# Kernel optimization log

Hardware: AMD Instinct MI355X
Metric: run time of the kernel (lower is better)

Reference implementation:

```python
import jax, jax.numpy as jnp
import numpy as np

FORGET_BIAS = 1.0  # TF BasicLSTMCell default


def _lstm_scan(xs, kernel, bias):
    """xs: [T, B, D]; kernel: [D+H, 4H]; bias: [4H]. Returns hs: [T, B, H]."""
    hidden = bias.shape[0] // 4
    batch = xs.shape[1]

    def step(carry, x):
        c, h = carry
        z = jnp.concatenate([x, h], axis=-1) @ kernel + bias
        i, j, f, o = jnp.split(z, 4, axis=-1)  # TF gate order: input, candidate, forget, output
        c_new = c * jax.nn.sigmoid(f + FORGET_BIAS) + jax.nn.sigmoid(i) * jnp.tanh(j)
        h_new = jnp.tanh(c_new) * jax.nn.sigmoid(o)
        return (c_new, h_new), h_new

    init = (jnp.zeros((batch, hidden), xs.dtype), jnp.zeros((batch, hidden), xs.dtype))
    _, hs = jax.lax.scan(step, init, xs)
    return hs


def setup_inputs() -> dict:
    key = jax.random.key(0)
    ks = jax.random.split(key, 8)
    B, T, D, H, V, L = 128, 512, 128, 128, 50000, 19
    return {
        "input_ids": jax.random.randint(ks[0], (B, T), 0, V, dtype=jnp.int32),
        "embedding_table": jax.random.normal(ks[1], (V, D), jnp.float32) * 0.02,
        "fw_kernel": jax.random.normal(ks[2], (D + H, 4 * H), jnp.float32) * 0.05,
        "fw_bias": jnp.zeros((4 * H,), jnp.float32),
        "bw_kernel": jax.random.normal(ks[3], (D + H, 4 * H), jnp.float32) * 0.05,
        "bw_bias": jnp.zeros((4 * H,), jnp.float32),
        "att_w": jax.random.normal(ks[4], (H,), jnp.float32) * 0.1,
        "fc_w": jax.random.normal(ks[5], (H, L), jnp.float32) * 0.1,
        "fc_b": jnp.zeros((L,), jnp.float32),
    }


def reference(input_ids, embedding_table, fw_kernel, fw_bias, bw_kernel, bw_bias, att_w, fc_w, fc_b):
    # Embedding lookup: [B, T, D]
    x = embedding_table[input_ids]
    xs = jnp.transpose(x, (1, 0, 2))  # [T, B, D] time-major for scan

    fw = jnp.transpose(_lstm_scan(xs, fw_kernel, fw_bias), (1, 0, 2))           # [B, T, H]
    bw = jnp.transpose(_lstm_scan(xs[::-1], bw_kernel, bw_bias)[::-1], (1, 0, 2))  # [B, T, H]

    Hsum = fw + bw                         # [B, T, H]
    M = jnp.tanh(Hsum)
    scores = jnp.einsum('bth,h->bt', M, att_w)
    alpha = jax.nn.softmax(scores, axis=-1)            # [B, T]
    r = jnp.einsum('bth,bt->bh', Hsum, alpha)          # attention-pooled [B, H]
    h_star = jnp.tanh(r)                               # keep_prob=1.0 -> dropout is identity

    logits = h_star @ fc_w + fc_b                      # [B, L]
    probabilities = jnp.argmax(jax.nn.softmax(logits, axis=-1), axis=1)
    predict_label_ids = jnp.argmax(logits, axis=1)
    l2_loss = 0.5 * (jnp.sum(fc_w * fc_w) + jnp.sum(fc_b * fc_b))  # tf.nn.l2_loss
    return logits, predict_label_ids, l2_loss, probabilities
```

## Files before the change

### kernel.cpp

```cpp
#include <hip/hip_runtime.h>

typedef unsigned short u16;
typedef unsigned int u32;
typedef short short8 __attribute__((ext_vector_type(8)));
typedef float f32x4 __attribute__((ext_vector_type(4)));

#define T_LEN 512
#define NCLS 19

#define L2E 1.4426950408889634f
#define TL2E 2.8853901617765067f

static __device__ __forceinline__ u16 f2bf(float f) {
  u32 u = __float_as_uint(f);
  u32 r = (u + 0x7FFFu + ((u >> 16) & 1u)) >> 16;
  return (u16)r;
}
static __device__ __forceinline__ float bf2f(u16 h) {
  return __uint_as_float(((u32)h) << 16);
}
static __device__ __forceinline__ float rcp_f(float x) { return __builtin_amdgcn_rcpf(x); }
static __device__ __forceinline__ float ex2(float x) { return __builtin_amdgcn_exp2f(x); }

__global__ __launch_bounds__(256) void k_embed(const int* __restrict__ ids,
                                               const float* __restrict__ table,
                                               u16* __restrict__ xs) {
  int i = blockIdx.x * 256 + threadIdx.x;
  int e = i * 4;
  int m = e >> 7;
  int col = e & 127;
  int t = m >> 7, b = m & 127;
  int id = ids[b * T_LEN + t];
  float4 v = *(const float4*)(table + (size_t)id * 128 + col);
  ushort4 o;
  o.x = f2bf(v.x); o.y = f2bf(v.y); o.z = f2bf(v.z); o.w = f2bf(v.w);
  *(ushort4*)(xs + (size_t)m * 128 + col) = o;
}

__global__ __launch_bounds__(256) void k_prep(const float* __restrict__ fw_k,
                                              const float* __restrict__ bw_k,
                                              const float* __restrict__ fw_b,
                                              const float* __restrict__ bw_b,
                                              u16* __restrict__ wt_bf,
                                              float* __restrict__ bias_pre) {
  int wg = blockIdx.x;
  int tid = threadIdx.x;
  if (wg < 1024) {
    int i = wg * 256 + tid;
    int n = i >> 8, k = i & 255;
    int dir = n >> 9, p = n & 511;
    int w = p >> 6, nt = (p >> 4) & 3, g4 = (p >> 2) & 3, q = p & 3;
    int u = w * 16 + g4 * 4 + nt;
    int j = q * 128 + u;
    float sc = (q == 1) ? TL2E : L2E;
    const float* K = dir ? bw_k : fw_k;
    wt_bf[i] = f2bf(K[k * 512 + j] * sc);
  } else {
    for (int uu = 0; uu < 4; uu++) {
      int n = uu * 256 + tid;
      int dir = n >> 9, p = n & 511;
      int w = p >> 6, nt = (p >> 4) & 3, g4 = (p >> 2) & 3, q = p & 3;
      int u = w * 16 + g4 * 4 + nt;
      int j = q * 128 + u;
      float sc = (q == 1) ? TL2E : L2E;
      float bv = (dir ? bw_b : fw_b)[j] + (q == 2 ? 1.0f : 0.0f);
      bias_pre[n] = bv * sc;
    }
  }
}

__global__ __launch_bounds__(512, 2) void k_lstm(const u16* __restrict__ wt_bf,
                                                 const float* __restrict__ bias_pre,
                                                 const u16* __restrict__ xs,
                                                 u16* __restrict__ hs_fw,
                                                 u16* __restrict__ hs_bw) {
  __shared__ u16 hbuf[2][4][144];
  __shared__ float zbuf[4][520];
  __shared__ float xstage[16][520];
  int tid = threadIdx.x;
  int wg = blockIdx.x;
  int dir = wg >> 5;
  int bb = (wg & 31) * 4;
  int w = tid >> 6, l = tid & 63;
  int cb = l & 15, g4 = l >> 4;
  int cbv = cb & 3;
  int so = cb >> 2;

  short8 wf[32];
#pragma unroll
  for (int n = 0; n < 4; n++) {
    const u16* wb = wt_bf + ((size_t)(dir * 512 + w * 64 + n * 16 + cb) * 256) + g4 * 8;
#pragma unroll
    for (int ks = 0; ks < 8; ks++)
      wf[n * 8 + ks] = *(const short8*)(wb + ks * 32);
  }
  f32x4 bias4[4];
#pragma unroll
  for (int n = 0; n < 4; n++)
    bias4[n] = *(const f32x4*)(bias_pre + dir * 512 + w * 64 + n * 16 + g4 * 4);

  int cbl = tid >> 7;
  int un = tid & 127;
  int p0 = (un >> 4) * 64 + (un & 3) * 16 + ((un >> 2) & 3) * 4;
  float c = 0.0f;

  int roff[4];
#pragma unroll
  for (int ks = 0; ks < 4; ks++)
    roff[ks] = cbv * 288 + ks * 64 + g4 * 16;
  int zoff = w * 64 + g4 * 4;
  int xcol = w * 256 + g4 * 16;

  u32* hz = (u32*)hbuf;
  hz[tid >= 512 ? 0 : tid] = 0;
  if (tid < 64) hz[512 + tid] = 0;
  __syncthreads();

  int t0a = dir ? (T_LEN - 1) : 0;
  int stp = dir ? -1 : 1;
  u16* hsout = dir ? hs_bw : hs_fw;
  long step1 = (long)stp * 16384;

  const u16* xb0 = xs + ((size_t)(t0a * 128 + bb + cbv) * 128) + g4 * 8;
  u16* ph = hsout + ((size_t)(t0a * 128 + bb + cbl) * 128) + un;

  short8 xblk[4];
  {
    const u16* p = xb0 + (long)so * step1;
#pragma unroll
    for (int ks = 0; ks < 4; ks++) xblk[ks] = *(const short8*)(p + ks * 32);
  }
#pragma unroll
  for (int n = 0; n < 4; n++) {
    f32x4 xacc = bias4[n];
    xacc = __builtin_amdgcn_mfma_f32_16x16x32_bf16(wf[n * 8 + 0], xblk[0], xacc, 0, 0, 0);
    xacc = __builtin_amdgcn_mfma_f32_16x16x32_bf16(wf[n * 8 + 1], xblk[1], xacc, 0, 0, 0);
    xacc = __builtin_amdgcn_mfma_f32_16x16x32_bf16(wf[n * 8 + 2], xblk[2], xacc, 0, 0, 0);
    xacc = __builtin_amdgcn_mfma_f32_16x16x32_bf16(wf[n * 8 + 3], xblk[3], xacc, 0, 0, 0);
    *(f32x4*)((char*)&xstage[cb][0] + xcol + n * 64) = xacc;
  }
  {
    const u16* p = xb0 + (long)(4 + so) * step1;
#pragma unroll
    for (int ks = 0; ks < 4; ks++) xblk[ks] = *(const short8*)(p + ks * 32);
  }
  asm volatile("s_waitcnt lgkmcnt(0)" ::: "memory");
  __builtin_amdgcn_s_barrier();
  asm volatile("" ::: "memory");

  for (int t = 0; t < T_LEN; t++) {
    int CUR = t & 1, NXT = CUR ^ 1;
    const char* hrow = (const char*)&hbuf[CUR][0][0];
    short8 hf0 = *(const short8*)(hrow + roff[0]);
    short8 hf1 = *(const short8*)(hrow + roff[1]);
    short8 hf2 = *(const short8*)(hrow + roff[2]);
    short8 hf3 = *(const short8*)(hrow + roff[3]);
#pragma unroll
    for (int n = 0; n < 4; n++) {
      f32x4 acc = {0.f, 0.f, 0.f, 0.f};
      acc = __builtin_amdgcn_mfma_f32_16x16x32_bf16(wf[n * 8 + 4], hf0, acc, 0, 0, 0);
      acc = __builtin_amdgcn_mfma_f32_16x16x32_bf16(wf[n * 8 + 5], hf1, acc, 0, 0, 0);
      acc = __builtin_amdgcn_mfma_f32_16x16x32_bf16(wf[n * 8 + 6], hf2, acc, 0, 0, 0);
      acc = __builtin_amdgcn_mfma_f32_16x16x32_bf16(wf[n * 8 + 7], hf3, acc, 0, 0, 0);
      if (cb < 4) *(f32x4*)&zbuf[cb][zoff + n * 16] = acc;
    }
    asm volatile("s_waitcnt lgkmcnt(0)" ::: "memory");
    __builtin_amdgcn_s_barrier();
    asm volatile("" ::: "memory");
    f32x4 zh = *(const f32x4*)&zbuf[cbl][p0];
    f32x4 zx = *(const f32x4*)&xstage[(t & 3) * 4 + cbl][p0];
    float z0 = zh[0] + zx[0];
    float z1 = zh[1] + zx[1];
    float z2 = zh[2] + zx[2];
    float z3 = zh[3] + zx[3];
    float A2 = ex2(-z0);
    float B2 = ex2(z1);
    float F2 = ex2(-z2);
    float O2 = ex2(-z3);
    float r1 = rcp_f((1.f + A2) * (1.f + B2));
    float rf = rcp_f(1.f + F2);
    float cn = fmaf(c, rf, (B2 - 1.f) * r1);
    c = cn;
    float C2 = ex2(cn * TL2E);
    float r2 = rcp_f((1.f + C2) * (1.f + O2));
    float hv = (C2 - 1.f) * r2;
    u16 hb16 = f2bf(hv);
    hbuf[NXT][cbl][un] = hb16;
    *ph = hb16;
    ph += step1;
    if ((t & 3) == 3 && t < 508) {
      asm volatile("s_waitcnt lgkmcnt(0)" ::: "memory");
      __builtin_amdgcn_s_barrier();
      asm volatile("" ::: "memory");
#pragma unroll
      for (int n = 0; n < 4; n++) {
        f32x4 xacc = bias4[n];
        xacc = __builtin_amdgcn_mfma_f32_16x16x32_bf16(wf[n * 8 + 0], xblk[0], xacc, 0, 0, 0);
        xacc = __builtin_amdgcn_mfma_f32_16x16x32_bf16(wf[n * 8 + 1], xblk[1], xacc, 0, 0, 0);
        xacc = __builtin_amdgcn_mfma_f32_16x16x32_bf16(wf[n * 8 + 2], xblk[2], xacc, 0, 0, 0);
        xacc = __builtin_amdgcn_mfma_f32_16x16x32_bf16(wf[n * 8 + 3], xblk[3], xacc, 0, 0, 0);
        *(f32x4*)((char*)&xstage[cb][0] + xcol + n * 64) = xacc;
      }
      int ts = t + 5 + so;
      if (ts > 511) ts = 511;
      const u16* p = xb0 + (long)ts * step1;
#pragma unroll
      for (int ks = 0; ks < 4; ks++) xblk[ks] = *(const short8*)(p + ks * 32);
    }
    asm volatile("s_waitcnt lgkmcnt(0)" ::: "memory");
    __builtin_amdgcn_s_barrier();
    asm volatile("" ::: "memory");
  }
}

__global__ __launch_bounds__(512) void k_attn(const u16* __restrict__ hsf,
                                              const u16* __restrict__ hsb,
                                              const float* __restrict__ att_w,
                                              const float* __restrict__ fc_w,
                                              const float* __restrict__ fc_b,
                                              float* __restrict__ out) {
  __shared__ float rsum[8][128];
  __shared__ float esums[8];
  __shared__ float hstar[128];
  __shared__ float lg[NCLS];
  int tid = threadIdx.x, b = blockIdx.x;
  int w = tid >> 6, l = tid & 63;
  float2 aw = *(const float2*)(att_w + 2 * l);
  float r0 = 0.f, r1 = 0.f, es = 0.f;
  for (int t = w; t < T_LEN; t += 8) {
    size_t o = ((size_t)t * 128 + b) * 128 + 2 * l;
    u32 vf = *(const u32*)(hsf + o);
    u32 vb = *(const u32*)(hsb + o);
    float h0 = bf2f((u16)vf) + bf2f((u16)vb);
    float h1 = bf2f((u16)(vf >> 16)) + bf2f((u16)(vb >> 16));
    float e0 = ex2(h0 * TL2E);
    float th0 = (e0 - 1.f) * rcp_f(e0 + 1.f);
    float e1 = ex2(h1 * TL2E);
    float th1 = (e1 - 1.f) * rcp_f(e1 + 1.f);
    float s = fmaf(th0, aw.x, th1 * aw.y);
#pragma unroll
    for (int o2 = 32; o2 >= 1; o2 >>= 1) s += __shfl_xor(s, o2, 64);
    float e = ex2(s * L2E);
    r0 = fmaf(e, h0, r0); r1 = fmaf(e, h1, r1); es += e;
  }
  rsum[w][2 * l] = r0;
  rsum[w][2 * l + 1] = r1;
  if (l == 0) esums[w] = es;
  __syncthreads();
  if (tid < 128) {
    float r = 0.f, et = 0.f;
#pragma unroll
    for (int i = 0; i < 8; i++) { r += rsum[i][tid]; et += esums[i]; }
    float rr = r / et;
    float e2 = ex2(rr * TL2E);
    hstar[tid] = (e2 - 1.f) * rcp_f(e2 + 1.f);
  }
  __syncthreads();
  if (tid < NCLS) {
    float acc = fc_b[tid];
#pragma unroll 4
    for (int hh = 0; hh < 128; hh++) acc = fmaf(hstar[hh], fc_w[hh * NCLS + tid], acc);
    out[b * NCLS + tid] = acc;
    lg[tid] = acc;
  }
  __syncthreads();
  if (tid == 0) {
    int best = 0; float bv = lg[0];
    for (int l2 = 1; l2 < NCLS; l2++)
      if (lg[l2] > bv) { bv = lg[l2]; best = l2; }
    out[2432 + b] = (float)best;
    out[2561 + b] = (float)best;
  }
}

__global__ __launch_bounds__(256) void k_l2(const float* __restrict__ fc_w,
                                            const float* __restrict__ fc_b,
                                            float* __restrict__ out) {
  __shared__ float red[256];
  int tid = threadIdx.x;
  float a = 0.f;
  for (int i = tid; i < 128 * NCLS; i += 256) a += fc_w[i] * fc_w[i];
  if (tid < NCLS) a += fc_b[tid] * fc_b[tid];
  red[tid] = a; __syncthreads();
  for (int s = 128; s >= 1; s >>= 1) {
    if (tid < s) red[tid] += red[tid + s];
    __syncthreads();
  }
  if (tid == 0) out[2560] = 0.5f * red[0];
}

extern "C" void kernel_launch(void* const* d_in, const int* in_sizes, int n_in,
                              void* d_out, int out_size, void* d_ws, size_t ws_size,
                              hipStream_t stream) {
  const int* ids = (const int*)d_in[0];
  const float* table = (const float*)d_in[1];
  const float* fw_k = (const float*)d_in[2];
  const float* fw_b = (const float*)d_in[3];
  const float* bw_k = (const float*)d_in[4];
  const float* bw_b = (const float*)d_in[5];
  const float* att_w = (const float*)d_in[6];
  const float* fc_w = (const float*)d_in[7];
  const float* fc_b = (const float*)d_in[8];
  float* out = (float*)d_out;
  char* ws = (char*)d_ws;

  u16* xs = (u16*)(ws + 0);
  u16* wt_bf = (u16*)(ws + 16777216);
  float* bias_pre = (float*)(ws + 17301504);
  u16* hs_fw = (u16*)(ws + 17305600);
  u16* hs_bw = (u16*)(ws + 34082816);

  hipLaunchKernelGGL(k_embed, dim3(8192), dim3(256), 0, stream, ids, table, xs);
  hipLaunchKernelGGL(k_prep, dim3(1025), dim3(256), 0, stream, fw_k, bw_k, fw_b, bw_b,
                     wt_bf, bias_pre);
  hipLaunchKernelGGL(k_lstm, dim3(64), dim3(512), 0, stream, wt_bf, bias_pre, xs,
                     hs_fw, hs_bw);
  hipLaunchKernelGGL(k_attn, dim3(128), dim3(512), 0, stream, hs_fw, hs_bw, att_w,
                     fc_w, fc_b, out);
  hipLaunchKernelGGL(k_l2, dim3(1), dim3(256), 0, stream, fc_w, fc_b, out);
}
```

Baseline: 438.5 us.

## Keep recurrent gate pre-activations in registers, removing zbuf round-trip and barrier

Each wave now computes all four gate tiles for the hidden columns and picks its own lane's result from registers, instead of writing z to shared zbuf and reading it back after a barrier. This drops one LDS store/load pair and one workgroup barrier per timestep on the serial recurrence critical path. The four MFMA chains are interleaved to hide their latency. In exchange every lane redundantly computes all 16 MFMAs and uses a select chain, which adds register pressure. The barrier is moved to follow the h write, and xstage padding is changed to 524.

```diff
diff --git a/kernel.cpp b/kernel.cpp
--- a/kernel.cpp
+++ b/kernel.cpp
@@ -75,8 +75,7 @@
                                                  u16* __restrict__ hs_fw,
                                                  u16* __restrict__ hs_bw) {
   __shared__ u16 hbuf[2][4][144];
-  __shared__ float zbuf[4][520];
-  __shared__ float xstage[16][520];
+  __shared__ float xstage[16][524];
   int tid = threadIdx.x;
   int wg = blockIdx.x;
   int dir = wg >> 5;
@@ -99,16 +98,13 @@
   for (int n = 0; n < 4; n++)
     bias4[n] = *(const f32x4*)(bias_pre + dir * 512 + w * 64 + n * 16 + g4 * 4);
 
-  int cbl = tid >> 7;
-  int un = tid & 127;
-  int p0 = (un >> 4) * 64 + (un & 3) * 16 + ((un >> 2) & 3) * 4;
   float c = 0.0f;
+  int u_so = w * 16 + g4 * 4 + so;
 
   int roff[4];
 #pragma unroll
   for (int ks = 0; ks < 4; ks++)
     roff[ks] = cbv * 288 + ks * 64 + g4 * 16;
-  int zoff = w * 64 + g4 * 4;
   int xcol = w * 256 + g4 * 16;
 
   u32* hz = (u32*)hbuf;
@@ -122,7 +118,7 @@
   long step1 = (long)stp * 16384;
 
   const u16* xb0 = xs + ((size_t)(t0a * 128 + bb + cbv) * 128) + g4 * 8;
-  u16* ph = hsout + ((size_t)(t0a * 128 + bb + cbl) * 128) + un;
+  u16* ph = hsout + ((size_t)(t0a * 128 + bb + cbv) * 128) + u_so;
 
   short8 xblk[4];
   {
@@ -155,20 +151,27 @@
     short8 hf1 = *(const short8*)(hrow + roff[1]);
     short8 hf2 = *(const short8*)(hrow + roff[2]);
     short8 hf3 = *(const short8*)(hrow + roff[3]);
-#pragma unroll
-    for (int n = 0; n < 4; n++) {
-      f32x4 acc = {0.f, 0.f, 0.f, 0.f};
-      acc = __builtin_amdgcn_mfma_f32_16x16x32_bf16(wf[n * 8 + 4], hf0, acc, 0, 0, 0);
-      acc = __builtin_amdgcn_mfma_f32_16x16x32_bf16(wf[n * 8 + 5], hf1, acc, 0, 0, 0);
-      acc = __builtin_amdgcn_mfma_f32_16x16x32_bf16(wf[n * 8 + 6], hf2, acc, 0, 0, 0);
-      acc = __builtin_amdgcn_mfma_f32_16x16x32_bf16(wf[n * 8 + 7], hf3, acc, 0, 0, 0);
-      if (cb < 4) *(f32x4*)&zbuf[cb][zoff + n * 16] = acc;
-    }
-    asm volatile("s_waitcnt lgkmcnt(0)" ::: "memory");
-    __builtin_amdgcn_s_barrier();
-    asm volatile("" ::: "memory");
-    f32x4 zh = *(const f32x4*)&zbuf[cbl][p0];
-    f32x4 zx = *(const f32x4*)&xstage[(t & 3) * 4 + cbl][p0];
+    f32x4 a0 = {0.f, 0.f, 0.f, 0.f}, a1 = a0, a2 = a0, a3 = a0;
+    a0 = __builtin_amdgcn_mfma_f32_16x16x32_bf16(wf[4],  hf0, a0, 0, 0, 0);
+    a1 = __builtin_amdgcn_mfma_f32_16x16x32_bf16(wf[12], hf0, a1, 0, 0, 0);
+    a2 = __builtin_amdgcn_mfma_f32_16x16x32_bf16(wf[20], hf0, a2, 0, 0, 0);
+    a3 = __builtin_amdgcn_mfma_f32_16x16x32_bf16(wf[28], hf0, a3, 0, 0, 0);
+    a0 = __builtin_amdgcn_mfma_f32_16x16x32_bf16(wf[5],  hf1, a0, 0, 0, 0);
+    a1 = __builtin_amdgcn_mfma_f32_16x16x32_bf16(wf[13], hf1, a1, 0, 0, 0);
+    a2 = __builtin_amdgcn_mfma_f32_16x16x32_bf16(wf[21], hf1, a2, 0, 0, 0);
+    a3 = __builtin_amdgcn_mfma_f32_16x16x32_bf16(wf[29], hf1, a3, 0, 0, 0);
+    a0 = __builtin_amdgcn_mfma_f32_16x16x32_bf16(wf[6],  hf2, a0, 0, 0, 0);
+    a1 = __builtin_amdgcn_mfma_f32_16x16x32_bf16(wf[14], hf2, a1, 0, 0, 0);
+    a2 = __builtin_amdgcn_mfma_f32_16x16x32_bf16(wf[22], hf2, a2, 0, 0, 0);
+    a3 = __builtin_amdgcn_mfma_f32_16x16x32_bf16(wf[30], hf2, a3, 0, 0, 0);
+    a0 = __builtin_amdgcn_mfma_f32_16x16x32_bf16(wf[7],  hf3, a0, 0, 0, 0);
+    a1 = __builtin_amdgcn_mfma_f32_16x16x32_bf16(wf[15], hf3, a1, 0, 0, 0);
+    a2 = __builtin_amdgcn_mfma_f32_16x16x32_bf16(wf[23], hf3, a2, 0, 0, 0);
+    a3 = __builtin_amdgcn_mfma_f32_16x16x32_bf16(wf[31], hf3, a3, 0, 0, 0);
+    f32x4 zA = (so & 2) ? a2 : a0;
+    f32x4 zB = (so & 2) ? a3 : a1;
+    f32x4 zh = (so & 1) ? zB : zA;
+    f32x4 zx = *(const f32x4*)&xstage[(t & 3) * 4 + cbv][w * 64 + so * 16 + g4 * 4];
     float z0 = zh[0] + zx[0];
     float z1 = zh[1] + zx[1];
     float z2 = zh[2] + zx[2];
@@ -185,13 +188,13 @@
     float r2 = rcp_f((1.f + C2) * (1.f + O2));
     float hv = (C2 - 1.f) * r2;
     u16 hb16 = f2bf(hv);
-    hbuf[NXT][cbl][un] = hb16;
+    hbuf[NXT][cbv][u_so] = hb16;
     *ph = hb16;
     ph += step1;
+    asm volatile("s_waitcnt lgkmcnt(0)" ::: "memory");
+    __builtin_amdgcn_s_barrier();
+    asm volatile("" ::: "memory");
     if ((t & 3) == 3 && t < 508) {
-      asm volatile("s_waitcnt lgkmcnt(0)" ::: "memory");
-      __builtin_amdgcn_s_barrier();
-      asm volatile("" ::: "memory");
 #pragma unroll
       for (int n = 0; n < 4; n++) {
         f32x4 xacc = bias4[n];
@@ -206,10 +209,10 @@
       const u16* p = xb0 + (long)ts * step1;
 #pragma unroll
       for (int ks = 0; ks < 4; ks++) xblk[ks] = *(const short8*)(p + ks * 32);
+      asm volatile("s_waitcnt lgkmcnt(0)" ::: "memory");
+      __builtin_amdgcn_s_barrier();
+      asm volatile("" ::: "memory");
     }
-    asm volatile("s_waitcnt lgkmcnt(0)" ::: "memory");
-    __builtin_amdgcn_s_barrier();
-    asm volatile("" ::: "memory");
   }
 }
 
```

Measured after the change: 356.5 us. 18.7% less time.
